# Optimization experiments

Measured on AMD Instinct MI355X. Metric: run time of the kernel, lower is better.

The kernel has to match this reference:

```python
import jax, jax.numpy as jnp
import numpy as np

B, T, V, E, H, DA, R, SC, AT = 128, 64, 32000, 300, 256, 128, 8, 32, 16
NUM_ROUTING = 3


def _lstm_dir(x, w_ih, w_hh, b, reverse):
    # x: [T, B, in]; torch LSTM gate order i, f, g, o
    Hh = w_hh.shape[1]

    def step(carry, xt):
        h, c = carry
        z = xt @ w_ih.T + h @ w_hh.T + b
        i, f, g, o = jnp.split(z, 4, axis=-1)
        c = jax.nn.sigmoid(f) * c + jax.nn.sigmoid(i) * jnp.tanh(g)
        h = jax.nn.sigmoid(o) * jnp.tanh(c)
        return (h, c), h

    init = (jnp.zeros((x.shape[1], Hh), x.dtype), jnp.zeros((x.shape[1], Hh), x.dtype))
    _, hs = jax.lax.scan(step, init, x, reverse=reverse)
    return hs


def setup_inputs():
    key = jax.random.key(0)
    ks = jax.random.split(key, 16)

    def g(k, shape, s=0.05):
        return jax.random.normal(k, shape, dtype=jnp.float32) * s

    return {
        "tokens": jax.random.randint(ks[0], (B, T), 0, V),
        "lengths": jnp.full((B,), T, dtype=jnp.int32),
        "embedding": g(ks[1], (V, E), 0.1),
        "w_ih_f0": g(ks[2], (4 * H, E)),
        "w_hh_f0": g(ks[3], (4 * H, H)),
        "b_f0": jnp.zeros((4 * H,), jnp.float32),
        "w_ih_b0": g(ks[4], (4 * H, E)),
        "w_hh_b0": g(ks[5], (4 * H, H)),
        "b_b0": jnp.zeros((4 * H,), jnp.float32),
        "w_ih_f1": g(ks[6], (4 * H, 2 * H)),
        "w_hh_f1": g(ks[7], (4 * H, H)),
        "b_f1": jnp.zeros((4 * H,), jnp.float32),
        "w_ih_b1": g(ks[8], (4 * H, 2 * H)),
        "w_hh_b1": g(ks[9], (4 * H, H)),
        "b_b1": jnp.zeros((4 * H,), jnp.float32),
        "ws1": g(ks[10], (DA, 2 * H)),
        "ws2": g(ks[11], (R, DA)),
        "caps_w": g(ks[12], (R, 2 * H, SC * AT)),
    }


def reference(tokens, lengths, embedding, w_ih_f0, w_hh_f0, b_f0, w_ih_b0, w_hh_b0, b_b0,
              w_ih_f1, w_hh_f1, b_f1, w_ih_b1, w_hh_b1, b_b1, ws1, ws2, caps_w):
    # Embedding lookup (all lengths == T, so packing is a no-op)
    x = embedding[tokens].transpose(1, 0, 2)  # [T, B, E]
    # 2-layer BiLSTM
    x1 = jnp.concatenate([
        _lstm_dir(x, w_ih_f0, w_hh_f0, b_f0, False),
        _lstm_dir(x, w_ih_b0, w_hh_b0, b_b0, True)], axis=-1)  # [T, B, 2H]
    outp = jnp.concatenate([
        _lstm_dir(x1, w_ih_f1, w_hh_f1, b_f1, False),
        _lstm_dir(x1, w_ih_b1, w_hh_b1, b_b1, True)], axis=-1)
    outp = outp.transpose(1, 0, 2)  # [B, T, 2H]
    # self-attention pooling (dropout is eval-mode identity)
    hbar = jnp.tanh(jnp.einsum('btu,du->btd', outp, ws1))
    attention = jnp.einsum('btd,rd->brt', hbar, ws2)            # [B, r, T]
    sent = jnp.einsum('brt,btu->bru', attention, outp)          # [B, r, 2H]
    # capsule votes: equals sum(input_tiled * capsule_weights, dim=2)
    votes = jnp.einsum('bru,ruo->bro', sent, caps_w).reshape(B, R, SC, AT)
    # dynamic routing
    logits = jnp.zeros((B, R, SC), votes.dtype)
    act = None
    for _ in range(NUM_ROUTING):
        route = jax.nn.softmax(logits, axis=2)
        preact = jnp.einsum('brc,brca->bca', route, votes)      # [B, SC, AT]
        norm = jnp.linalg.norm(preact, axis=2, keepdims=True)
        n2 = norm * norm
        act = preact / norm * (n2 / (0.5 + n2))                 # squash
        logits = logits + jnp.einsum('brca,bca->brc', votes, act)
    return jnp.linalg.norm(act, axis=-1)  # [B, SC] class logits
```

## Files before the change

kernel.cpp:

```cpp
#include <hip/hip_runtime.h>
#include <hip/hip_bf16.h>


typedef __attribute__((ext_vector_type(8))) short bf16x8;
typedef __attribute__((ext_vector_type(4))) float f32x4;

__device__ __forceinline__ float sigf(float x) { return 1.0f / (1.0f + __expf(-x)); }
__device__ __forceinline__ float tanhf_fast(float x) { return 1.0f - 2.0f / (__expf(2.0f * x) + 1.0f); }

__global__ void k_transpose(const float* __restrict__ w0, const float* __restrict__ w1,
                            const float* __restrict__ w2, const float* __restrict__ w3,
                            float* __restrict__ wt)
{
    __shared__ float tile[32][33];
    const float* W = (blockIdx.z == 0) ? w0 : (blockIdx.z == 1) ? w1 : (blockIdx.z == 2) ? w2 : w3;
    float* Wt = wt + (size_t)blockIdx.z * 256 * 1024;
    const int j0 = blockIdx.x * 32, k0 = blockIdx.y * 32;
    const int tx = threadIdx.x, ty = threadIdx.y;
    #pragma unroll
    for (int i = 0; i < 32; i += 8)
        tile[ty + i][tx] = W[(size_t)(j0 + ty + i) * 256 + (k0 + tx)];
    __syncthreads();
    #pragma unroll
    for (int i = 0; i < 32; i += 8)
        Wt[(size_t)(k0 + ty + i) * 1024 + (j0 + tx)] = tile[tx][ty + i];
}

__global__ void k_zero(int* __restrict__ p, int n)
{
    const int i = blockIdx.x * blockDim.x + threadIdx.x;
    if (i < n) p[i] = 0;
}

__global__ __launch_bounds__(256) void k_mgemm(
    const float* __restrict__ A, int lda, const int* __restrict__ tokens,
    const float* __restrict__ W0, const float* __restrict__ W1, int ldw,
    const float* __restrict__ bias0, const float* __restrict__ bias1,
    float* __restrict__ C, int ldc, int Kin, int Kp, int act_tanh)
{
    __shared__ unsigned short lAh[128 * 40];
    __shared__ unsigned short lAl[128 * 40];
    __shared__ unsigned short lBh[128 * 40];
    __shared__ unsigned short lBl[128 * 40];

    const int tid = threadIdx.x;
    const int m0 = blockIdx.x * 128;
    const int n0 = blockIdx.y * 128;
    const int w  = tid >> 6, l = tid & 63;
    const int wm = (w >> 1) * 64, wn = (w & 1) * 64;
    const int lr = l & 15, lk = (l >> 4) * 8;

    int srow[2], sk8[2];
    const float* arow[2];
    const float* wrow[2];
    #pragma unroll
    for (int p = 0; p < 2; ++p) {
        const int chunk = tid + p * 256;
        srow[p] = chunk >> 2;
        sk8[p]  = (chunk & 3) * 8;
        const int am = m0 + srow[p];
        if (tokens) {
            const int t = am >> 7, b = am & 127;
            arow[p] = A + (size_t)tokens[b * 64 + t] * lda;
        } else {
            arow[p] = A + (size_t)am * lda;
        }
        const int wnr = n0 + srow[p];
        wrow[p] = (wnr < 1024) ? (W0 + (size_t)wnr * ldw)
                               : (W1 + (size_t)(wnr - 1024) * ldw);
    }

    f32x4 acc[4][4];
    #pragma unroll
    for (int i = 0; i < 4; ++i)
        #pragma unroll
        for (int j = 0; j < 4; ++j)
            acc[i][j] = (f32x4){0.f, 0.f, 0.f, 0.f};

    float fa[2][8], fw[2][8];
    #pragma unroll
    for (int p = 0; p < 2; ++p) {
        const int k0 = sk8[p];
        if (k0 + 7 < Kin) {
            const float4 a0 = *(const float4*)(arow[p] + k0);
            const float4 a1 = *(const float4*)(arow[p] + k0 + 4);
            fa[p][0]=a0.x; fa[p][1]=a0.y; fa[p][2]=a0.z; fa[p][3]=a0.w;
            fa[p][4]=a1.x; fa[p][5]=a1.y; fa[p][6]=a1.z; fa[p][7]=a1.w;
            const float4 b0 = *(const float4*)(wrow[p] + k0);
            const float4 b1 = *(const float4*)(wrow[p] + k0 + 4);
            fw[p][0]=b0.x; fw[p][1]=b0.y; fw[p][2]=b0.z; fw[p][3]=b0.w;
            fw[p][4]=b1.x; fw[p][5]=b1.y; fw[p][6]=b1.z; fw[p][7]=b1.w;
        } else {
            #pragma unroll
            for (int j = 0; j < 8; ++j) {
                fa[p][j] = (k0 + j < Kin) ? arow[p][k0 + j] : 0.0f;
                fw[p][j] = (k0 + j < Kin) ? wrow[p][k0 + j] : 0.0f;
            }
        }
    }

    for (int kt = 0; kt < Kp; kt += 32) {
        #pragma unroll
        for (int p = 0; p < 2; ++p) {
            const int la = srow[p] * 40 + sk8[p];
            ushort hA[8], lA[8], hW[8], lW[8];
            #pragma unroll
            for (int j = 0; j < 8; ++j) {
                __hip_bfloat16 bh = __float2bfloat16(fa[p][j]);
                const float fh = __bfloat162float(bh);
                __hip_bfloat16 bl = __float2bfloat16(fa[p][j] - fh);
                hA[j] = *(ushort*)&bh; lA[j] = *(ushort*)&bl;
                __hip_bfloat16 wh = __float2bfloat16(fw[p][j]);
                const float fwh = __bfloat162float(wh);
                __hip_bfloat16 wl = __float2bfloat16(fw[p][j] - fwh);
                hW[j] = *(ushort*)&wh; lW[j] = *(ushort*)&wl;
            }
            *(bf16x8*)&lAh[la] = *(bf16x8*)hA;
            *(bf16x8*)&lAl[la] = *(bf16x8*)lA;
            *(bf16x8*)&lBh[la] = *(bf16x8*)hW;
            *(bf16x8*)&lBl[la] = *(bf16x8*)lW;
        }
        __syncthreads();
        if (kt + 32 < Kp) {
            #pragma unroll
            for (int p = 0; p < 2; ++p) {
                const int k0 = kt + 32 + sk8[p];
                if (k0 + 7 < Kin) {
                    const float4 a0 = *(const float4*)(arow[p] + k0);
                    const float4 a1 = *(const float4*)(arow[p] + k0 + 4);
                    fa[p][0]=a0.x; fa[p][1]=a0.y; fa[p][2]=a0.z; fa[p][3]=a0.w;
                    fa[p][4]=a1.x; fa[p][5]=a1.y; fa[p][6]=a1.z; fa[p][7]=a1.w;
                    const float4 b0 = *(const float4*)(wrow[p] + k0);
                    const float4 b1 = *(const float4*)(wrow[p] + k0 + 4);
                    fw[p][0]=b0.x; fw[p][1]=b0.y; fw[p][2]=b0.z; fw[p][3]=b0.w;
                    fw[p][4]=b1.x; fw[p][5]=b1.y; fw[p][6]=b1.z; fw[p][7]=b1.w;
                } else {
                    #pragma unroll
                    for (int j = 0; j < 8; ++j) {
                        fa[p][j] = (k0 + j < Kin) ? arow[p][k0 + j] : 0.0f;
                        fw[p][j] = (k0 + j < Kin) ? wrow[p][k0 + j] : 0.0f;
                    }
                }
            }
        }
        bf16x8 ah[4], al[4], bh[4], bl[4];
        #pragma unroll
        for (int f = 0; f < 4; ++f) {
            const int ra = (wm + f * 16 + lr) * 40 + lk;
            const int rb = (wn + f * 16 + lr) * 40 + lk;
            ah[f] = *(const bf16x8*)&lAh[ra];
            al[f] = *(const bf16x8*)&lAl[ra];
            bh[f] = *(const bf16x8*)&lBh[rb];
            bl[f] = *(const bf16x8*)&lBl[rb];
        }
        #pragma unroll
        for (int fm = 0; fm < 4; ++fm)
            #pragma unroll
            for (int fn = 0; fn < 4; ++fn) {
                acc[fm][fn] = __builtin_amdgcn_mfma_f32_16x16x32_bf16(ah[fm], bh[fn], acc[fm][fn], 0, 0, 0);
                acc[fm][fn] = __builtin_amdgcn_mfma_f32_16x16x32_bf16(ah[fm], bl[fn], acc[fm][fn], 0, 0, 0);
                acc[fm][fn] = __builtin_amdgcn_mfma_f32_16x16x32_bf16(al[fm], bh[fn], acc[fm][fn], 0, 0, 0);
            }
        __syncthreads();
    }
    #pragma unroll
    for (int fm = 0; fm < 4; ++fm)
        #pragma unroll
        for (int fn = 0; fn < 4; ++fn) {
            const int col = n0 + wn + fn * 16 + lr;
            const float bv = (col < 1024) ? (bias0 ? bias0[col] : 0.f)
                                          : (bias1 ? bias1[col - 1024] : 0.f);
            #pragma unroll
            for (int j = 0; j < 4; ++j) {
                const int row = m0 + wm + fm * 16 + (l >> 4) * 4 + j;
                float x = acc[fm][fn][j] + bv;
                if (act_tanh) x = tanhf_fast(x);
                C[(size_t)row * ldc + col] = x;
            }
        }
}

__global__ __launch_bounds__(256) void k_gemm(
    const float* __restrict__ A, int lda, const int* __restrict__ tokens,
    const float* __restrict__ W0, const float* __restrict__ W1, int nsplit, int ldw,
    const float* __restrict__ bias0, const float* __restrict__ bias1,
    float* __restrict__ C, int ldc, int K, int transb, int act_tanh,
    long long sA, long long sW, long long sC)
{
    __shared__ float As[32][128];
    __shared__ float Ws[32][128];
    A  += (size_t)blockIdx.z * (size_t)sA;
    W0 += (size_t)blockIdx.z * (size_t)sW;
    C  += (size_t)blockIdx.z * (size_t)sC;
    const int tid = threadIdx.x;
    const int m0 = blockIdx.x * 128;
    const int n0 = blockIdx.y * 128;

    const int srow = tid >> 1;
    const int kh   = (tid & 1) * 16;
    const int am = m0 + srow;
    const float* arow;
    if (tokens) {
        const int t = am >> 7, b = am & 127;
        arow = A + (size_t)tokens[b * 64 + t] * lda;
    } else {
        arow = A + (size_t)am * lda;
    }
    const int wn = n0 + srow;
    const float* wrow = (wn < nsplit) ? (W0 + (size_t)wn * ldw)
                                      : (W1 + (size_t)(wn - nsplit) * ldw);
    const int kw = tid >> 3;
    const int n8 = (tid & 7) * 16;

    const int tm4 = (tid & 15) * 4;
    const int tn4 = (tid >> 4) * 4;
    float acc[8][8] = {};
    float4 ra[4], rw[4];

    const int nt = (K + 31) / 32;

    #pragma unroll
    for (int j = 0; j < 4; ++j) {
        const int k = kh + j * 4;
        if (k + 3 < K) ra[j] = *(const float4*)(arow + k);
        else {
            float t0 = (k + 0 < K) ? arow[k + 0] : 0.f;
            float t1 = (k + 1 < K) ? arow[k + 1] : 0.f;
            float t2 = (k + 2 < K) ? arow[k + 2] : 0.f;
            float t3 = (k + 3 < K) ? arow[k + 3] : 0.f;
            ra[j] = make_float4(t0, t1, t2, t3);
        }
    }
    if (transb) {
        #pragma unroll
        for (int j = 0; j < 4; ++j) {
            const int k = kh + j * 4;
            if (k + 3 < K) rw[j] = *(const float4*)(wrow + k);
            else {
                float t0 = (k + 0 < K) ? wrow[k + 0] : 0.f;
                float t1 = (k + 1 < K) ? wrow[k + 1] : 0.f;
                float t2 = (k + 2 < K) ? wrow[k + 2] : 0.f;
                float t3 = (k + 3 < K) ? wrow[k + 3] : 0.f;
                rw[j] = make_float4(t0, t1, t2, t3);
            }
        }
    } else {
        const float* src = (kw < K) ? (W0 + (size_t)kw * ldw + n0 + n8) : W0;
        #pragma unroll
        for (int j = 0; j < 4; ++j)
            rw[j] = (kw < K) ? *(const float4*)(src + j * 4) : make_float4(0, 0, 0, 0);
    }

    for (int tile = 0; tile < nt; ++tile) {
        #pragma unroll
        for (int j = 0; j < 4; ++j) {
            As[kh + j * 4 + 0][srow] = ra[j].x;
            As[kh + j * 4 + 1][srow] = ra[j].y;
            As[kh + j * 4 + 2][srow] = ra[j].z;
            As[kh + j * 4 + 3][srow] = ra[j].w;
        }
        if (transb) {
            #pragma unroll
            for (int j = 0; j < 4; ++j) {
                Ws[kh + j * 4 + 0][srow] = rw[j].x;
                Ws[kh + j * 4 + 1][srow] = rw[j].y;
                Ws[kh + j * 4 + 2][srow] = rw[j].z;
                Ws[kh + j * 4 + 3][srow] = rw[j].w;
            }
        } else {
            #pragma unroll
            for (int j = 0; j < 4; ++j)
                *(float4*)&Ws[kw][n8 + j * 4] = rw[j];
        }
        __syncthreads();
        if (tile + 1 < nt) {
            const int kb = (tile + 1) * 32;
            #pragma unroll
            for (int j = 0; j < 4; ++j) {
                const int k = kb + kh + j * 4;
                if (k + 3 < K) ra[j] = *(const float4*)(arow + k);
                else {
                    float t0 = (k + 0 < K) ? arow[k + 0] : 0.f;
                    float t1 = (k + 1 < K) ? arow[k + 1] : 0.f;
                    float t2 = (k + 2 < K) ? arow[k + 2] : 0.f;
                    float t3 = (k + 3 < K) ? arow[k + 3] : 0.f;
                    ra[j] = make_float4(t0, t1, t2, t3);
                }
            }
            if (transb) {
                #pragma unroll
                for (int j = 0; j < 4; ++j) {
                    const int k = kb + kh + j * 4;
                    if (k + 3 < K) rw[j] = *(const float4*)(wrow + k);
                    else {
                        float t0 = (k + 0 < K) ? wrow[k + 0] : 0.f;
                        float t1 = (k + 1 < K) ? wrow[k + 1] : 0.f;
                        float t2 = (k + 2 < K) ? wrow[k + 2] : 0.f;
                        float t3 = (k + 3 < K) ? wrow[k + 3] : 0.f;
                        rw[j] = make_float4(t0, t1, t2, t3);
                    }
                }
            } else {
                const int k = kb + kw;
                const float* src = (k < K) ? (W0 + (size_t)k * ldw + n0 + n8) : W0;
                #pragma unroll
                for (int j = 0; j < 4; ++j)
                    rw[j] = (k < K) ? *(const float4*)(src + j * 4) : make_float4(0, 0, 0, 0);
            }
        }
        #pragma unroll 8
        for (int kk = 0; kk < 32; ++kk) {
            const float4 a0 = *(const float4*)&As[kk][tm4];
            const float4 a1 = *(const float4*)&As[kk][tm4 + 64];
            const float4 b0 = *(const float4*)&Ws[kk][tn4];
            const float4 b1 = *(const float4*)&Ws[kk][tn4 + 64];
            const float av[8] = {a0.x, a0.y, a0.z, a0.w, a1.x, a1.y, a1.z, a1.w};
            const float bv[8] = {b0.x, b0.y, b0.z, b0.w, b1.x, b1.y, b1.z, b1.w};
            #pragma unroll
            for (int i = 0; i < 8; ++i)
                #pragma unroll
                for (int j = 0; j < 8; ++j)
                    acc[i][j] += av[i] * bv[j];
        }
        __syncthreads();
    }
    const int half = (n0 >= nsplit) ? 1 : 0;
    const float* bp = half ? bias1 : bias0;
    const int nl = n0 - (half ? nsplit : 0);
    #pragma unroll
    for (int i = 0; i < 8; ++i) {
        const int row = m0 + tm4 + (i >> 2) * 64 + (i & 3);
        #pragma unroll
        for (int jh = 0; jh < 2; ++jh) {
            float v[4];
            #pragma unroll
            for (int j = 0; j < 4; ++j) {
                float x = acc[i][jh * 4 + j];
                if (bp) x += bp[nl + tn4 + jh * 64 + j];
                if (act_tanh) x = tanhf_fast(x);
                v[j] = x;
            }
            *(float4*)(C + (size_t)row * ldc + n0 + tn4 + jh * 64) =
                make_float4(v[0], v[1], v[2], v[3]);
        }
    }
}

__global__ __launch_bounds__(512, 2) void k_scan9(
    const float* __restrict__ Zin, const float* __restrict__ WtF,
    const float* __restrict__ WtB, float* __restrict__ outbuf,
    int bt_layout, unsigned int* __restrict__ hx32, int* __restrict__ flags,
    int bx_base)
{
    __shared__ __align__(16) unsigned short hbh[16 * 264];
    __shared__ __align__(16) unsigned short hbl[16 * 264];
    __shared__ float zbuf[8 * 16 * 17];

    const int bx  = blockIdx.x + bx_base;
    const int g   = bx & 15;
    const int s   = bx >> 4;
    const int dir = g >> 3;
    const int qg  = g & 7;
    const int tid = threadIdx.x;
    const int w   = tid >> 6;
    const int l   = tid & 63;
    const int lr  = l & 15;
    const int lk8 = (l >> 4) * 8;
    const float* __restrict__ Wt = dir ? WtB : WtF;

    const int colg = (w >> 1) * 256 + s * 32 + (w & 1) * 16 + lr;
    bf16x8 wbh[8], wbl[8];
    #pragma unroll
    for (int kf = 0; kf < 8; ++kf) {
        ushort ph[8], pl[8];
        #pragma unroll
        for (int j = 0; j < 8; ++j) {
            const int k = kf * 32 + lk8 + j;
            const float v = Wt[(size_t)k * 1024 + colg];
            __hip_bfloat16 bh = __float2bfloat16(v);
            __hip_bfloat16 bl = __float2bfloat16(v - __bfloat162float(bh));
            ph[j] = *(ushort*)&bh; pl[j] = *(ushort*)&bl;
        }
        wbh[kf] = *(bf16x8*)ph;
        wbl[kf] = *(bf16x8*)pl;
    }

    const int bi  = tid >> 5;
    const int di  = tid & 31;
    const int gb  = qg * 16 + bi;
    const int dim = s * 32 + di;
    float c_state = 0.0f;
    const int fbase = g * 64;
    const int st_base = (tid >> 5) * 256 + (tid & 31) * 8;
    const int st_lds  = (tid >> 5) * 264 + (tid & 31) * 8;

    for (int tt = 0; tt < 64; ++tt) {
        const int t = dir ? (63 - tt) : tt;
        const float* zr = Zin + (size_t)(t * 128 + gb) * 2048 + dir * 1024 + dim;
        const float z0 = zr[0], z1 = zr[256], z2 = zr[512], z3 = zr[768];
        if (tt > 0) {
            if (tid == 0) {
                while (__hip_atomic_load(&flags[fbase + tt - 1], __ATOMIC_RELAXED,
                                         __HIP_MEMORY_SCOPE_AGENT) < 8)
                    __builtin_amdgcn_s_sleep(1);
            }
            __syncthreads();
            {
                const unsigned long long* hs64 = (const unsigned long long*)
                    (hx32 + ((size_t)(((tt - 1) & 1) * 16 + g)) * 4096 + st_base);
                unsigned int hp[4], lp[4];
                #pragma unroll
                for (int j = 0; j < 4; ++j) {
                    const unsigned long long q = __hip_atomic_load(&hs64[j], __ATOMIC_RELAXED,
                                                                   __HIP_MEMORY_SCOPE_AGENT);
                    const unsigned int w0 = (unsigned int)q;
                    const unsigned int w1 = (unsigned int)(q >> 32);
                    hp[j] = (w0 >> 16) | (w1 & 0xFFFF0000u);
                    lp[j] = (w0 & 0xFFFFu) | (w1 << 16);
                }
                *(uint4*)&hbh[st_lds] = make_uint4(hp[0], hp[1], hp[2], hp[3]);
                *(uint4*)&hbl[st_lds] = make_uint4(lp[0], lp[1], lp[2], lp[3]);
            }
            __syncthreads();
            f32x4 acc = (f32x4){0.f, 0.f, 0.f, 0.f};
            #pragma unroll
            for (int kf = 0; kf < 8; ++kf) {
                const int ao = lr * 264 + kf * 32 + lk8;
                const bf16x8 ah = *(const bf16x8*)&hbh[ao];
                const bf16x8 al = *(const bf16x8*)&hbl[ao];
                acc = __builtin_amdgcn_mfma_f32_16x16x32_bf16(ah, wbh[kf], acc, 0, 0, 0);
                acc = __builtin_amdgcn_mfma_f32_16x16x32_bf16(ah, wbl[kf], acc, 0, 0, 0);
                acc = __builtin_amdgcn_mfma_f32_16x16x32_bf16(al, wbh[kf], acc, 0, 0, 0);
            }
            #pragma unroll
            for (int j = 0; j < 4; ++j)
                zbuf[(w * 16 + (l >> 4) * 4 + j) * 17 + lr] = acc[j];
            __syncthreads();
        } else {
            for (int i = tid; i < 2176; i += 512) zbuf[i] = 0.0f;
            __syncthreads();
        }
        {
            const int dh = di >> 4, dl = di & 15;
            const float zi = zbuf[((0 * 2 + dh) * 16 + bi) * 17 + dl] + z0;
            const float zf = zbuf[((1 * 2 + dh) * 16 + bi) * 17 + dl] + z1;
            const float zg = zbuf[((2 * 2 + dh) * 16 + bi) * 17 + dl] + z2;
            const float zo = zbuf[((3 * 2 + dh) * 16 + bi) * 17 + dl] + z3;
            c_state = sigf(zf) * c_state + sigf(zi) * tanhf_fast(zg);
            const float h = sigf(zo) * tanhf_fast(c_state);
            const int row = bt_layout ? (gb * 64 + t) : (t * 128 + gb);
            outbuf[(size_t)row * 512 + dir * 256 + dim] = h;
            __hip_bfloat16 bh = __float2bfloat16(h);
            __hip_bfloat16 bl = __float2bfloat16(h - __bfloat162float(bh));
            const unsigned int pk = ((unsigned int)(*(ushort*)&bh) << 16) | (*(ushort*)&bl);
            __hip_atomic_store(
                &hx32[((size_t)((tt & 1) * 16 + g)) * 4096 + bi * 256 + dim],
                pk, __ATOMIC_RELAXED, __HIP_MEMORY_SCOPE_AGENT);
        }
        __syncthreads();
        if (tid == 0)
            __hip_atomic_fetch_add(&flags[fbase + tt], 1, __ATOMIC_RELAXED,
                                   __HIP_MEMORY_SCOPE_AGENT);
    }
}

__global__ __launch_bounds__(256) void k_attnpool(
    const float* __restrict__ hbar, const float* __restrict__ outp,
    const float* __restrict__ ws2, float* __restrict__ sent)
{
    __shared__ float hb[64][132];
    __shared__ float w2[8][128];
    __shared__ float att[8][64];
    const int b = blockIdx.x, tid = threadIdx.x;
    for (int i = tid; i < 1024; i += 256) ((float*)w2)[i] = ws2[i];
    const float* hsrc = hbar + (size_t)b * 64 * 128;
    for (int i = tid; i < 2048; i += 256) {
        const int row = i >> 5, d4 = (i & 31) << 2;
        *(float4*)&hb[row][d4] = *(const float4*)(hsrc + row * 128 + d4);
    }
    __syncthreads();
    for (int p = tid; p < 512; p += 256) {
        const int r = p >> 6, t = p & 63;
        float s = 0.0f;
        #pragma unroll 8
        for (int d = 0; d < 128; d += 4) {
            const float4 x = *(const float4*)&hb[t][d];
            const float4 y = *(const float4*)&w2[r][d];
            s += x.x * y.x + x.y * y.y + x.z * y.z + x.w * y.w;
        }
        att[r][t] = s;
    }
    __syncthreads();
    const float* ob = outp + (size_t)b * 64 * 512;
    float s0[8] = {}, s1[8] = {};
    for (int t = 0; t < 64; ++t) {
        const float v0 = ob[t * 512 + tid];
        const float v1 = ob[t * 512 + 256 + tid];
        #pragma unroll
        for (int r = 0; r < 8; ++r) {
            const float a = att[r][t];
            s0[r] += a * v0; s1[r] += a * v1;
        }
    }
    #pragma unroll
    for (int r = 0; r < 8; ++r) {
        sent[((size_t)b * 8 + r) * 512 + tid]       = s0[r];
        sent[((size_t)b * 8 + r) * 512 + 256 + tid] = s1[r];
    }
}

__global__ __launch_bounds__(512) void k_routing(
    const float* __restrict__ votes, float* __restrict__ out)
{
    __shared__ float v[8][32][16];
    __shared__ float logits[8][32];
    __shared__ float route[8][32];
    const int b = blockIdx.x, tid = threadIdx.x;
    const float* vb = votes + (size_t)b * 4096;
    for (int i = tid; i < 4096; i += 512) ((float*)v)[i] = vb[i];
    if (tid < 256) ((float*)logits)[tid] = 0.0f;
    __syncthreads();
    const int c = tid >> 4, a = tid & 15;
    float n2 = 0.0f;
    for (int it = 0; it < 3; ++it) {
        if (tid < 256) {
            const int r = tid >> 5, cc = tid & 31;
            const float l = logits[r][cc];
            float mx = l;
            #pragma unroll
            for (int m = 1; m < 32; m <<= 1) mx = fmaxf(mx, __shfl_xor(mx, m));
            const float e = __expf(l - mx);
            float sm = e;
            #pragma unroll
            for (int m = 1; m < 32; m <<= 1) sm += __shfl_xor(sm, m);
            route[r][cc] = e / sm;
        }
        __syncthreads();
        float pa = 0.0f;
        #pragma unroll
        for (int r = 0; r < 8; ++r) pa += route[r][c] * v[r][c][a];
        n2 = pa * pa;
        #pragma unroll
        for (int m = 1; m < 16; m <<= 1) n2 += __shfl_xor(n2, m);
        const float nrm = sqrtf(n2);
        const float av = pa * (nrm / (0.5f + n2));
        if (it < 2) {
            #pragma unroll
            for (int r = 0; r < 8; ++r) {
                float u = v[r][c][a] * av;
                #pragma unroll
                for (int m = 1; m < 16; m <<= 1) u += __shfl_xor(u, m);
                if (a == 0) logits[r][c] += u;
            }
        }
        __syncthreads();
    }
    if (a == 0) out[b * 32 + c] = n2 / (0.5f + n2);
}

static void launch_scan(const float* Z, const float* wf, const float* wb,
                        float* ob, int bt, unsigned int* hx32, int* fl,
                        hipStream_t stream)
{
    int base0 = 0;
    void* args[] = {(void*)&Z, (void*)&wf, (void*)&wb, (void*)&ob,
                    (void*)&bt, (void*)&hx32, (void*)&fl, (void*)&base0};
    if (hipLaunchCooperativeKernel((const void*)k_scan9, dim3(128), dim3(512),
                                   args, 0, stream) != hipSuccess) {
        k_scan9<<<dim3(128), 512, 0, stream>>>(Z, wf, wb, ob, bt, hx32, fl, 0);
    }
}

extern "C" void kernel_launch(void* const* d_in, const int* in_sizes, int n_in,
                              void* d_out, int out_size, void* d_ws, size_t ws_size,
                              hipStream_t stream) {
    (void)in_sizes; (void)n_in; (void)out_size; (void)ws_size;
    const int*   tokens  = (const int*)d_in[0];
    const float* emb     = (const float*)d_in[2];
    const float* w_ih_f0 = (const float*)d_in[3];
    const float* w_hh_f0 = (const float*)d_in[4];
    const float* b_f0    = (const float*)d_in[5];
    const float* w_ih_b0 = (const float*)d_in[6];
    const float* w_hh_b0 = (const float*)d_in[7];
    const float* b_b0    = (const float*)d_in[8];
    const float* w_ih_f1 = (const float*)d_in[9];
    const float* w_hh_f1 = (const float*)d_in[10];
    const float* b_f1    = (const float*)d_in[11];
    const float* w_ih_b1 = (const float*)d_in[12];
    const float* w_hh_b1 = (const float*)d_in[13];
    const float* b_b1    = (const float*)d_in[14];
    const float* ws1     = (const float*)d_in[15];
    const float* ws2     = (const float*)d_in[16];
    const float* caps    = (const float*)d_in[17];

    float* wsf  = (float*)d_ws;
    float* Wt   = wsf;
    float* Z    = Wt   + 4 * 262144;
    float* x1   = Z    + 16777216;
    float* outp = x1   + 4194304;
    float* hbar = outp + 4194304;
    float* sent = hbar + 1048576;
    float* vote = sent + 524288;
    unsigned int* hx32 = (unsigned int*)(vote + 524288);
    int*   flags = (int*)(hx32 + 131072);
    float* out  = (float*)d_out;

    k_zero<<<dim3(32), 256, 0, stream>>>(flags, 8192);
    k_transpose<<<dim3(32, 8, 4), dim3(32, 8), 0, stream>>>(w_hh_f0, w_hh_b0, w_hh_f1, w_hh_b1, Wt);
    k_mgemm<<<dim3(64, 16), 256, 0, stream>>>(
        emb, 300, tokens, w_ih_f0, w_ih_b0, 300, b_f0, b_b0, Z, 2048, 300, 320, 0);
    launch_scan(Z, Wt, Wt + 262144, x1, 0, hx32, flags, stream);
    k_mgemm<<<dim3(64, 16), 256, 0, stream>>>(
        x1, 512, (const int*)nullptr, w_ih_f1, w_ih_b1, 512, b_f1, b_b1, Z, 2048, 512, 512, 0);
    launch_scan(Z, Wt + 2 * 262144, Wt + 3 * 262144, outp, 1, hx32, flags + 4096, stream);
    k_mgemm<<<dim3(64, 1), 256, 0, stream>>>(
        outp, 512, (const int*)nullptr, ws1, ws1, 512,
        (const float*)nullptr, (const float*)nullptr, hbar, 128, 512, 512, 1);
    k_attnpool<<<dim3(128), 256, 0, stream>>>(hbar, outp, ws2, sent);
    k_gemm<<<dim3(1, 4, 8), 256, 0, stream>>>(
        sent, 4096, (const int*)nullptr, caps, (const float*)nullptr, 1 << 30, 512,
        (const float*)nullptr, (const float*)nullptr,
        vote, 4096, 512, 0, 0, 512LL, 262144LL, 512LL);
    k_routing<<<dim3(128), 512, 0, stream>>>(vote, out);
}
```

Baseline: 579.0 us.

## Remap LSTM scan MFMA columns so gates combine via shuffles, cutting barriers

```diff
diff --git a/kernel.cpp b/kernel.cpp
--- a/kernel.cpp
+++ b/kernel.cpp
@@ -346,7 +346,7 @@
     }
 }
 
-__global__ __launch_bounds__(512, 2) void k_scan9(
+__global__ __launch_bounds__(512, 2) void k_scan10(
     const float* __restrict__ Zin, const float* __restrict__ WtF,
     const float* __restrict__ WtB, float* __restrict__ outbuf,
     int bt_layout, unsigned int* __restrict__ hx32, int* __restrict__ flags,
@@ -354,21 +354,24 @@
 {
     __shared__ __align__(16) unsigned short hbh[16 * 264];
     __shared__ __align__(16) unsigned short hbl[16 * 264];
-    __shared__ float zbuf[8 * 16 * 17];
+    __shared__ __align__(16) float zlds[16 * 132];
 
     const int bx  = blockIdx.x + bx_base;
-    const int g   = bx & 15;
+    const int gid = bx & 15;
     const int s   = bx >> 4;
-    const int dir = g >> 3;
-    const int qg  = g & 7;
+    const int dir = gid >> 3;
+    const int qg  = gid & 7;
     const int tid = threadIdx.x;
     const int w   = tid >> 6;
     const int l   = tid & 63;
     const int lr  = l & 15;
-    const int lk8 = (l >> 4) * 8;
+    const int rg  = l >> 4;
+    const int lk8 = rg * 8;
+    const int gt  = lr >> 2;
+    const int d   = lr & 3;
     const float* __restrict__ Wt = dir ? WtB : WtF;
 
-    const int colg = (w >> 1) * 256 + s * 32 + (w & 1) * 16 + lr;
+    const int colg = gt * 256 + s * 32 + w * 4 + d;
     bf16x8 wbh[8], wbl[8];
     #pragma unroll
     for (int kf = 0; kf < 8; ++kf) {
@@ -385,44 +388,42 @@
         wbl[kf] = *(bf16x8*)pl;
     }
 
-    const int bi  = tid >> 5;
-    const int di  = tid & 31;
-    const int gb  = qg * 16 + bi;
-    const int dim = s * 32 + di;
-    float c_state = 0.0f;
-    const int fbase = g * 64;
     const int st_base = (tid >> 5) * 256 + (tid & 31) * 8;
     const int st_lds  = (tid >> 5) * 264 + (tid & 31) * 8;
+    const int zrow = tid >> 5;
+    const int zseg = (tid >> 3) & 3;
+    const int zf4  = (tid & 7) * 4;
+    const int fbase = gid * 64;
+
+    float c_state[4] = {0.f, 0.f, 0.f, 0.f};
 
     for (int tt = 0; tt < 64; ++tt) {
         const int t = dir ? (63 - tt) : tt;
-        const float* zr = Zin + (size_t)(t * 128 + gb) * 2048 + dir * 1024 + dim;
-        const float z0 = zr[0], z1 = zr[256], z2 = zr[512], z3 = zr[768];
+        const float4 zv = *(const float4*)(Zin +
+            (size_t)(t * 128 + qg * 16 + zrow) * 2048 + dir * 1024 + zseg * 256 + s * 32 + zf4);
         if (tt > 0) {
-            if (tid == 0) {
-                while (__hip_atomic_load(&flags[fbase + tt - 1], __ATOMIC_RELAXED,
-                                         __HIP_MEMORY_SCOPE_AGENT) < 8)
-                    __builtin_amdgcn_s_sleep(1);
-            }
-            __syncthreads();
-            {
-                const unsigned long long* hs64 = (const unsigned long long*)
-                    (hx32 + ((size_t)(((tt - 1) & 1) * 16 + g)) * 4096 + st_base);
-                unsigned int hp[4], lp[4];
-                #pragma unroll
-                for (int j = 0; j < 4; ++j) {
-                    const unsigned long long q = __hip_atomic_load(&hs64[j], __ATOMIC_RELAXED,
-                                                                   __HIP_MEMORY_SCOPE_AGENT);
-                    const unsigned int w0 = (unsigned int)q;
-                    const unsigned int w1 = (unsigned int)(q >> 32);
-                    hp[j] = (w0 >> 16) | (w1 & 0xFFFF0000u);
-                    lp[j] = (w0 & 0xFFFFu) | (w1 << 16);
-                }
-                *(uint4*)&hbh[st_lds] = make_uint4(hp[0], hp[1], hp[2], hp[3]);
-                *(uint4*)&hbl[st_lds] = make_uint4(lp[0], lp[1], lp[2], lp[3]);
-            }
-            __syncthreads();
-            f32x4 acc = (f32x4){0.f, 0.f, 0.f, 0.f};
+            while (__hip_atomic_load(&flags[fbase + tt - 1], __ATOMIC_RELAXED,
+                                     __HIP_MEMORY_SCOPE_AGENT) < 8)
+                __builtin_amdgcn_s_sleep(1);
+            const unsigned long long* hs64 = (const unsigned long long*)
+                (hx32 + ((size_t)(((tt - 1) & 1) * 16 + gid)) * 4096 + st_base);
+            unsigned int hp[4], lp[4];
+            #pragma unroll
+            for (int j = 0; j < 4; ++j) {
+                const unsigned long long q = __hip_atomic_load(&hs64[j], __ATOMIC_RELAXED,
+                                                               __HIP_MEMORY_SCOPE_AGENT);
+                const unsigned int w0 = (unsigned int)q;
+                const unsigned int w1 = (unsigned int)(q >> 32);
+                hp[j] = (w0 >> 16) | (w1 & 0xFFFF0000u);
+                lp[j] = (w0 & 0xFFFFu) | (w1 << 16);
+            }
+            *(uint4*)&hbh[st_lds] = make_uint4(hp[0], hp[1], hp[2], hp[3]);
+            *(uint4*)&hbl[st_lds] = make_uint4(lp[0], lp[1], lp[2], lp[3]);
+        }
+        *(float4*)&zlds[zrow * 132 + zseg * 32 + zf4] = zv;
+        __syncthreads();
+        f32x4 acc = (f32x4){0.f, 0.f, 0.f, 0.f};
+        if (tt > 0) {
             #pragma unroll
             for (int kf = 0; kf < 8; ++kf) {
                 const int ao = lr * 264 + kf * 32 + lk8;
@@ -432,30 +433,31 @@
                 acc = __builtin_amdgcn_mfma_f32_16x16x32_bf16(ah, wbl[kf], acc, 0, 0, 0);
                 acc = __builtin_amdgcn_mfma_f32_16x16x32_bf16(al, wbh[kf], acc, 0, 0, 0);
             }
-            #pragma unroll
-            for (int j = 0; j < 4; ++j)
-                zbuf[(w * 16 + (l >> 4) * 4 + j) * 17 + lr] = acc[j];
-            __syncthreads();
-        } else {
-            for (int i = tid; i < 2176; i += 512) zbuf[i] = 0.0f;
-            __syncthreads();
-        }
-        {
-            const int dh = di >> 4, dl = di & 15;
-            const float zi = zbuf[((0 * 2 + dh) * 16 + bi) * 17 + dl] + z0;
-            const float zf = zbuf[((1 * 2 + dh) * 16 + bi) * 17 + dl] + z1;
-            const float zg = zbuf[((2 * 2 + dh) * 16 + bi) * 17 + dl] + z2;
-            const float zo = zbuf[((3 * 2 + dh) * 16 + bi) * 17 + dl] + z3;
-            c_state = sigf(zf) * c_state + sigf(zi) * tanhf_fast(zg);
-            const float h = sigf(zo) * tanhf_fast(c_state);
-            const int row = bt_layout ? (gb * 64 + t) : (t * 128 + gb);
-            outbuf[(size_t)row * 512 + dir * 256 + dim] = h;
-            __hip_bfloat16 bh = __float2bfloat16(h);
-            __hip_bfloat16 bl = __float2bfloat16(h - __bfloat162float(bh));
-            const unsigned int pk = ((unsigned int)(*(ushort*)&bh) << 16) | (*(ushort*)&bl);
-            __hip_atomic_store(
-                &hx32[((size_t)((tt & 1) * 16 + g)) * 4096 + bi * 256 + dim],
-                pk, __ATOMIC_RELAXED, __HIP_MEMORY_SCOPE_AGENT);
+        }
+        #pragma unroll
+        for (int j = 0; j < 4; ++j) {
+            const float zt = acc[j] + zlds[(rg * 4 + j) * 132 + gt * 32 + w * 4 + d];
+            const float v4  = __shfl_xor(zt, 4);
+            const float v8  = __shfl_xor(zt, 8);
+            const float v12 = __shfl_xor(zt, 12);
+            const float zi = (gt == 0) ? zt : (gt == 1) ? v4 : (gt == 2) ? v8 : v12;
+            const float zf = (gt == 1) ? zt : (gt == 0) ? v4 : (gt == 3) ? v8 : v12;
+            const float zg = (gt == 2) ? zt : (gt == 3) ? v4 : (gt == 0) ? v8 : v12;
+            const float zo = (gt == 3) ? zt : (gt == 2) ? v4 : (gt == 1) ? v8 : v12;
+            c_state[j] = sigf(zf) * c_state[j] + sigf(zi) * tanhf_fast(zg);
+            const float h = sigf(zo) * tanhf_fast(c_state[j]);
+            if (gt == 0) {
+                const int bglob = qg * 16 + rg * 4 + j;
+                const int dim = s * 32 + w * 4 + d;
+                const int row = bt_layout ? (bglob * 64 + t) : (t * 128 + bglob);
+                outbuf[(size_t)row * 512 + dir * 256 + dim] = h;
+                __hip_bfloat16 bh = __float2bfloat16(h);
+                __hip_bfloat16 bl = __float2bfloat16(h - __bfloat162float(bh));
+                const unsigned int pk = ((unsigned int)(*(ushort*)&bh) << 16) | (*(ushort*)&bl);
+                __hip_atomic_store(
+                    &hx32[((size_t)((tt & 1) * 16 + gid)) * 4096 + (rg * 4 + j) * 256 + dim],
+                    pk, __ATOMIC_RELAXED, __HIP_MEMORY_SCOPE_AGENT);
+            }
         }
         __syncthreads();
         if (tid == 0)
@@ -565,9 +567,9 @@
     int base0 = 0;
     void* args[] = {(void*)&Z, (void*)&wf, (void*)&wb, (void*)&ob,
                     (void*)&bt, (void*)&hx32, (void*)&fl, (void*)&base0};
-    if (hipLaunchCooperativeKernel((const void*)k_scan9, dim3(128), dim3(512),
+    if (hipLaunchCooperativeKernel((const void*)k_scan10, dim3(128), dim3(512),
                                    args, 0, stream) != hipSuccess) {
-        k_scan9<<<dim3(128), 512, 0, stream>>>(Z, wf, wb, ob, bt, hx32, fl, 0);
+        k_scan10<<<dim3(128), 512, 0, stream>>>(Z, wf, wb, ob, bt, hx32, fl, 0);
     }
 }
 
```

Measured after the change: 757.7 us. 30.9% more time.
